# Optimization experiments

Hardware: AMD Instinct MI355X
Metric: run time of the kernel (lower is better)

Reference implementation:

```python
import jax, jax.numpy as jnp
import numpy as np

B, N, F = 64, 512, 30          # batch, pf candidates, raw features
NDIM0, NDIM = 2, 4             # coord dims: layer0 uses 2, rest use n_dim_gnn=4
NOUT, NLAYERS = 64, 5          # GNN layer width / count
NDENSE = 128
BN_EPS = 1e-3                  # keras BatchNormalization default epsilon


def setup_inputs() -> dict:
    key = jax.random.key(0)
    ks = jax.random.split(key, 20)
    xx = jax.random.normal(ks[0], (B, N, F), jnp.float32)
    # validity mask: first L_b candidates valid
    lengths = jax.random.randint(ks[1], (B,), N // 4, N + 1)
    valid = (jnp.arange(N)[None, :] < lengths[:, None]).astype(jnp.float32)
    pt = jax.random.randint(ks[2], (B, N), 0, 8).astype(jnp.float32)
    pvq = jax.random.randint(ks[3], (B, N), 0, 8).astype(jnp.float32)
    fpv = jax.random.randint(ks[4], (B, N), 0, 4).astype(jnp.float32)
    xx = xx.at[:, :, 0].set(valid).at[:, :, 27].set(pt).at[:, :, 28].set(pvq).at[:, :, 29].set(fpv)
    g = lambda k, s, sc=0.05: jax.random.normal(k, s, jnp.float32) * sc
    d_in0 = 33  # 2+2+2 embeddings + 27 float features
    return {
        "xx": xx,
        "emb1": g(ks[5], (8, 2), 0.5),
        "emb2": g(ks[6], (8, 2), 0.5),
        "emb3": g(ks[7], (4, 2), 0.5),
        "A0": g(ks[8], ((d_in0 + 1) * 2 - 1, NOUT)),   # [67,64]
        "b0": g(ks[9], (NOUT,)),
        "A_rest": g(ks[10], (NLAYERS - 1, (NOUT + 1) * 2 - 1, NOUT)),  # [4,129,64]
        "b_rest": g(ks[11], (NLAYERS - 1, NOUT)),
        "bn_gamma": jnp.ones((NLAYERS, NOUT), jnp.float32),
        "bn_beta": jnp.zeros((NLAYERS, NOUT), jnp.float32),
        "dW0": g(ks[12], (N * NOUT, NDENSE), 0.01),
        "db0": g(ks[13], (NDENSE,)),
        "dW1": g(ks[14], (NDENSE, NDENSE)),
        "db1": g(ks[15], (NDENSE,)),
        "dbn_gamma": jnp.ones((2, NDENSE), jnp.float32),
        "dbn_beta": jnp.zeros((2, NDENSE), jnp.float32),
        "W2": g(ks[16], (NDENSE, 2)),
        "b2": g(ks[17], (2,)),
    }


def _bn(x, g, b):
    # inference BatchNorm with moving_mean=0, moving_var=1 (initial stats)
    return g * x * (1.0 / jnp.sqrt(1.0 + BN_EPS)) + b


def _gnn_layer(x, mask, n_dim, A, b):
    # x: [B,N,Fin], mask: [B,N]. Original builds [B,N,N,Fin+1] via tile/reshape;
    # algebraically the reduction over senders i factorizes:
    #   ss_feat[b,j] = x[b,j] * mask[b,j] * sum_i exp(-10*d_ij)
    #   ss_last[b,j] = mask[b,j] * sum_i d_ij * exp(-10*d_ij)
    c = x[..., -n_dim:]
    diff = c[:, :, None, :] - c[:, None, :, :]      # [B,N,N,n_dim]
    dist = jnp.sum(diff * diff, axis=-1)            # [B,N,N] squared distance
    w = jnp.exp(-10.0 * dist)
    S = jnp.sum(w, axis=1)                          # [B,N] per receiver j
    T = jnp.sum(dist * w, axis=1)                   # [B,N]
    ss_feat = x * (mask * S)[..., None] - x         # subtract concat(x, 0)
    ss_last = (mask * T)[..., None]
    xcat = jnp.concatenate([x, ss_feat, ss_last], axis=-1)  # [B,N,2*Fin+1]
    return (xcat @ A + b) * mask[..., None]


def _forward(xx, emb1, emb2, emb3, A0, b0, A_rest, b_rest, bn_gamma, bn_beta,
             dW0, db0, dW1, db1, dbn_gamma, dbn_beta, W2, b2):
    mask = xx[:, :, 0]
    e1 = emb1[jnp.abs(xx[:, :, 27]).astype(jnp.int32)]
    e2 = emb2[jnp.abs(xx[:, :, 28]).astype(jnp.int32)]
    e3 = emb3[jnp.abs(xx[:, :, 29]).astype(jnp.int32)]
    x = jnp.concatenate([e1, e2, e3, xx[:, :, :27]], axis=-1)  # [B,N,33]
    x = jnp.tanh(_bn(_gnn_layer(x, mask, NDIM0, A0, b0), bn_gamma[0], bn_beta[0]))
    for k in range(NLAYERS - 1):
        x = _gnn_layer(x, mask, NDIM, A_rest[k], b_rest[k])
        x = jnp.tanh(_bn(x, bn_gamma[k + 1], bn_beta[k + 1]))
    x = x.reshape(B, N * NOUT)
    x = jax.nn.sigmoid(_bn(x @ dW0 + db0, dbn_gamma[0], dbn_beta[0]))
    x = jax.nn.sigmoid(_bn(x @ dW1 + db1, dbn_gamma[1], dbn_beta[1]))
    x = x @ W2 + b2                                  # [B,2]
    # mode == 'dm': concat zeros on the right
    return jnp.concatenate([x, jnp.zeros((B, 2), x.dtype)], axis=1)


def reference(xx, emb1, emb2, emb3, A0, b0, A_rest, b_rest, bn_gamma, bn_beta,
              dW0, db0, dW1, db1, dbn_gamma, dbn_beta, W2, b2):
    return _forward(xx, emb1, emb2, emb3, A0, b0, A_rest, b_rest, bn_gamma, bn_beta,
                    dW0, db0, dW1, db1, dbn_gamma, dbn_beta, W2, b2)
```

## Files before the change

kernel.cpp:

```cpp
#include <hip/hip_runtime.h>
#include <math.h>

#define B_ 64
#define N_ 512
#define R_ (B_*N_)
#define INV_S 0.9995003746877732f

__device__ __forceinline__ float fast_tanh(float y){
  return 1.f - 2.f*__builtin_amdgcn_rcpf(1.f + __expf(2.f*y));
}
__device__ __forceinline__ float fast_sigmoid(float v){
  return __builtin_amdgcn_rcpf(1.f + __expf(-v));
}

template<int L0>
__global__ __launch_bounds__(512, 4) void gnn_layer(
    const float* __restrict__ xx, const float* __restrict__ xin,
    const float4* __restrict__ cin, const float* __restrict__ A,
    const float* __restrict__ bias, const float* __restrict__ gamma,
    const float* __restrict__ beta,
    const float* __restrict__ emb1, const float* __restrict__ emb2,
    const float* __restrict__ emb3,
    const float* __restrict__ maskb,
    float* __restrict__ maskout,
    float4* __restrict__ cout,
    float* __restrict__ xout)
{
  constexpr int KP = L0 ? 36 : 64;
  constexpr int K  = L0 ? 33 : 64;
  __shared__ float alo[KP*64];
  __shared__ float ahi[KP*64];
  __shared__ float xl[L0 ? 64*36 : 4];
  __shared__ float spart[512], tpart[512];
  __shared__ float scl[64], tcl[64], ml[64];

  int tid = threadIdx.x;
  int jc = blockIdx.x;
  int b  = blockIdx.y;
  int rbase = b*N_, jloc = jc*64;

  if constexpr (L0){
    for (int idx = tid; idx < KP*64; idx += 512){
      int f = idx >> 6;
      alo[idx] = (f < K) ? A[idx] : 0.f;
      ahi[idx] = (f < K) ? A[(size_t)K*64 + idx] : 0.f;
    }
  } else {
    const float4* A4 = (const float4*)A;
    float4* alo4 = (float4*)alo;
    float4* ahi4 = (float4*)ahi;
    for (int idx = tid; idx < 1024; idx += 512){
      alo4[idx] = A4[idx];
      ahi4[idx] = A4[1024 + idx];
    }
  }

  if constexpr (L0){
    if (tid < 64){
      int r = rbase + jloc + tid;
      const float* row = xx + (size_t)r*30;
      float v[30];
#pragma unroll
      for (int i=0;i<30;i++) v[i] = row[i];
      int i1 = (int)fabsf(v[27]);
      int i2 = (int)fabsf(v[28]);
      int i3 = (int)fabsf(v[29]);
      float* o = &xl[tid*36];
      o[0]=emb1[i1*2+0]; o[1]=emb1[i1*2+1];
      o[2]=emb2[i2*2+0]; o[3]=emb2[i2*2+1];
      o[4]=emb3[i3*2+0]; o[5]=emb3[i3*2+1];
#pragma unroll
      for (int i=0;i<27;i++) o[6+i] = v[i];
      o[33]=0.f; o[34]=0.f; o[35]=0.f;
      ml[tid] = v[0];
      maskout[r] = v[0];
    }
  } else {
    if (tid < 64) ml[tid] = maskb[rbase + jloc + tid];
  }

  {
    int jj = tid & 63, ic = tid >> 6;
    float Ss = 0.f, Ts = 0.f;
    if constexpr (L0){
      const float* xb = xx + (size_t)rbase*30;
      float cjx = xb[(jloc+jj)*30 + 25];
      float cjy = xb[(jloc+jj)*30 + 26];
      int base = ic*64;
#pragma unroll 8
      for (int i=0;i<64;i++){
        float cix = xb[(base+i)*30 + 25];
        float ciy = xb[(base+i)*30 + 26];
        float d0 = cjx-cix, d1 = cjy-ciy;
        float dist = d0*d0 + d1*d1;
        float w = __expf(-10.f*dist);
        Ss += w; Ts += dist*w;
      }
    } else {
      const float4* cb = cin + rbase;
      float4 cj = cb[jloc + jj];
      int base = ic*64;
#pragma unroll 8
      for (int i=0;i<64;i++){
        float4 ci = cb[base+i];
        float d0 = cj.x-ci.x, d1 = cj.y-ci.y, d2 = cj.z-ci.z, d3 = cj.w-ci.w;
        float dist = d0*d0 + d1*d1 + d2*d2 + d3*d3;
        float w = __expf(-10.f*dist);
        Ss += w; Ts += dist*w;
      }
    }
    spart[tid] = Ss;
    tpart[tid] = Ts;
  }
  __syncthreads();

  if (tid < 64){
    float S = 0.f, T = 0.f;
#pragma unroll
    for (int c=0;c<8;c++){
      S += spart[tid + 64*c];
      T += tpart[tid + 64*c];
    }
    float m = ml[tid];
    scl[tid] = m*S - 1.f;
    tcl[tid] = m*T;
  }
  __syncthreads();

  int cg = tid & 15, rg = tid >> 4;
  int o0 = cg*4, lr0 = rg*2;
  const float* xb2 = xin + (size_t)(rbase + jloc)*64;
  float4 acc1[2], acc2[2];
#pragma unroll
  for (int rr=0;rr<2;rr++){
    acc1[rr] = make_float4(0.f,0.f,0.f,0.f);
    acc2[rr] = make_float4(0.f,0.f,0.f,0.f);
  }
#pragma unroll 2
  for (int kc = 0; kc < KP; kc += 4){
    float4 a1[4], a2[4], xv[2];
#pragma unroll
    for (int uu=0;uu<4;uu++){
      a1[uu] = *(const float4*)&alo[(kc+uu)*64 + o0];
      a2[uu] = *(const float4*)&ahi[(kc+uu)*64 + o0];
    }
#pragma unroll
    for (int rr=0;rr<2;rr++){
      if constexpr (L0) xv[rr] = *(const float4*)&xl[(lr0+rr)*36 + kc];
      else              xv[rr] = *(const float4*)&xb2[(lr0+rr)*64 + kc];
    }
#pragma unroll
    for (int uu=0;uu<4;uu++){
#pragma unroll
      for (int rr=0;rr<2;rr++){
        float xu = ((const float*)&xv[rr])[uu];
        acc1[rr].x = fmaf(xu, a1[uu].x, acc1[rr].x);
        acc1[rr].y = fmaf(xu, a1[uu].y, acc1[rr].y);
        acc1[rr].z = fmaf(xu, a1[uu].z, acc1[rr].z);
        acc1[rr].w = fmaf(xu, a1[uu].w, acc1[rr].w);
        acc2[rr].x = fmaf(xu, a2[uu].x, acc2[rr].x);
        acc2[rr].y = fmaf(xu, a2[uu].y, acc2[rr].y);
        acc2[rr].z = fmaf(xu, a2[uu].z, acc2[rr].z);
        acc2[rr].w = fmaf(xu, a2[uu].w, acc2[rr].w);
      }
    }
  }

  float4 alast = *(const float4*)&A[(size_t)2*K*64 + o0];
  float4 bo = *(const float4*)&bias[o0];
  float4 go = *(const float4*)&gamma[o0];
  float4 be = *(const float4*)&beta[o0];
#pragma unroll
  for (int rr=0;rr<2;rr++){
    int lr = lr0 + rr;
    int r = rbase + jloc + lr;
    float sc = scl[lr], tc = tcl[lr], m = ml[lr];
    float4 v;
    v.x = (acc1[rr].x + sc*acc2[rr].x + tc*alast.x + bo.x)*m;
    v.y = (acc1[rr].y + sc*acc2[rr].y + tc*alast.y + bo.y)*m;
    v.z = (acc1[rr].z + sc*acc2[rr].z + tc*alast.z + bo.z)*m;
    v.w = (acc1[rr].w + sc*acc2[rr].w + tc*alast.w + bo.w)*m;
    float4 t;
    t.x = fast_tanh(go.x*(v.x*INV_S) + be.x);
    t.y = fast_tanh(go.y*(v.y*INV_S) + be.y);
    t.z = fast_tanh(go.z*(v.z*INV_S) + be.z);
    t.w = fast_tanh(go.w*(v.w*INV_S) + be.w);
    *(float4*)&xout[(size_t)r*64 + o0] = t;
    if (cout && cg == 15) cout[r] = t;
  }
}

__global__ __launch_bounds__(256) void dense0_partial(
    const float* __restrict__ X, const float* __restrict__ W,
    float* __restrict__ partial)
{
  __shared__ float xt[64*32];
  __shared__ float wt[32*128];
  int tid = threadIdx.x;
  int k0 = blockIdx.x*128;
  int og = (tid & 15)*8;
  int rg = (tid >> 4)*4;
  float acc[4][8];
#pragma unroll
  for (int a=0;a<4;a++)
#pragma unroll
    for (int u=0;u<8;u++) acc[a][u]=0.f;
  for (int kt = 0; kt < 128; kt += 32){
    __syncthreads();
    for (int idx = tid; idx < 512; idx += 256){
      int r = idx >> 3, kq = idx & 7;
      *(float4*)&xt[r*32 + kq*4] =
          *(const float4*)&X[(size_t)r*32768 + k0 + kt + kq*4];
    }
    {
      const float4* Wc = (const float4*)&W[(size_t)(k0+kt)*128];
      float4* wt4 = (float4*)wt;
      for (int idx = tid; idx < 1024; idx += 256) wt4[idx] = Wc[idx];
    }
    __syncthreads();
#pragma unroll 4
    for (int k=0;k<32;k++){
      float4 w0 = *(const float4*)&wt[k*128 + og];
      float4 w1 = *(const float4*)&wt[k*128 + og + 4];
      float xs[4];
#pragma unroll
      for (int rr=0;rr<4;rr++) xs[rr] = xt[(rg+rr)*32 + k];
#pragma unroll
      for (int rr=0;rr<4;rr++){
        acc[rr][0] = fmaf(xs[rr], w0.x, acc[rr][0]);
        acc[rr][1] = fmaf(xs[rr], w0.y, acc[rr][1]);
        acc[rr][2] = fmaf(xs[rr], w0.z, acc[rr][2]);
        acc[rr][3] = fmaf(xs[rr], w0.w, acc[rr][3]);
        acc[rr][4] = fmaf(xs[rr], w1.x, acc[rr][4]);
        acc[rr][5] = fmaf(xs[rr], w1.y, acc[rr][5]);
        acc[rr][6] = fmaf(xs[rr], w1.z, acc[rr][6]);
        acc[rr][7] = fmaf(xs[rr], w1.w, acc[rr][7]);
      }
    }
  }
  float* pb = partial + (size_t)blockIdx.x*8192;
#pragma unroll
  for (int rr=0;rr<4;rr++){
    *(float4*)&pb[(rg+rr)*128 + og]     = *(float4*)&acc[rr][0];
    *(float4*)&pb[(rg+rr)*128 + og + 4] = *(float4*)&acc[rr][4];
  }
}

__global__ __launch_bounds__(256) void dense_head(
    const float* __restrict__ partial,
    const float* __restrict__ db0, const float* __restrict__ dg0,
    const float* __restrict__ dbb0,
    const float* __restrict__ dW1, const float* __restrict__ db1,
    const float* __restrict__ dg1, const float* __restrict__ dbb1,
    const float* __restrict__ W2, const float* __restrict__ b2,
    float* __restrict__ out)
{
  __shared__ float sred[256];
  __shared__ float h[128];
  __shared__ float red0[128], red1[128];
  int tid = threadIdx.x;
  int b = blockIdx.x;
  int o = tid & 127, ph = tid >> 7;
  float s = 0.f;
#pragma unroll 16
  for (int p = ph*128; p < ph*128+128; p++)
    s += partial[(size_t)p*8192 + b*128 + o];
  sred[tid] = s;
  __syncthreads();
  if (tid < 128){
    float sum = sred[tid] + sred[tid+128];
    float v = dg0[tid]*((sum + db0[tid])*INV_S) + dbb0[tid];
    h[tid] = fast_sigmoid(v);
  }
  __syncthreads();
  if (tid < 128){
    float acc = 0.f;
#pragma unroll 8
    for (int k=0;k<128;k++) acc = fmaf(h[k], dW1[k*128 + tid], acc);
    float v = dg1[tid]*((acc + db1[tid])*INV_S) + dbb1[tid];
    float h1 = fast_sigmoid(v);
    red0[tid] = h1 * W2[tid*2+0];
    red1[tid] = h1 * W2[tid*2+1];
  }
  __syncthreads();
  for (int st=64; st>0; st>>=1){
    if (tid < st){ red0[tid] += red0[tid+st]; red1[tid] += red1[tid+st]; }
    __syncthreads();
  }
  if (tid == 0){
    out[b*4+0] = red0[0] + b2[0];
    out[b*4+1] = red1[0] + b2[1];
    out[b*4+2] = 0.f;
    out[b*4+3] = 0.f;
  }
}

extern "C" void kernel_launch(void* const* d_in, const int* in_sizes, int n_in,
                              void* d_out, int out_size, void* d_ws, size_t ws_size,
                              hipStream_t stream)
{
  const float* xx   = (const float*)d_in[0];
  const float* emb1 = (const float*)d_in[1];
  const float* emb2 = (const float*)d_in[2];
  const float* emb3 = (const float*)d_in[3];
  const float* A0   = (const float*)d_in[4];
  const float* b0   = (const float*)d_in[5];
  const float* Ar   = (const float*)d_in[6];
  const float* br   = (const float*)d_in[7];
  const float* bng  = (const float*)d_in[8];
  const float* bnb  = (const float*)d_in[9];
  const float* dW0  = (const float*)d_in[10];
  const float* db0  = (const float*)d_in[11];
  const float* dW1  = (const float*)d_in[12];
  const float* db1  = (const float*)d_in[13];
  const float* dbg  = (const float*)d_in[14];
  const float* dbb  = (const float*)d_in[15];
  const float* W2   = (const float*)d_in[16];
  const float* b2   = (const float*)d_in[17];

  float* ws = (float*)d_ws;
  float*  xA      = ws;
  float*  xB      = xA + (size_t)R_*64;
  float*  partial = xB + (size_t)R_*64;
  float*  maskb   = partial + (size_t)256*8192;
  float4* cb0     = (float4*)(maskb + R_);
  float4* cb1     = cb0 + R_;

  dim3 lgrid(8, 64);
  gnn_layer<1><<<lgrid, 512, 0, stream>>>(
      xx, nullptr, nullptr, A0, b0, bng, bnb, emb1, emb2, emb3,
      nullptr, maskb, cb1, xA);
  gnn_layer<0><<<lgrid, 512, 0, stream>>>(
      xx, xA, cb1, Ar + (size_t)0*129*64, br + 0*64, bng + 64, bnb + 64,
      emb1, emb2, emb3, maskb, nullptr, cb0, xB);
  gnn_layer<0><<<lgrid, 512, 0, stream>>>(
      xx, xB, cb0, Ar + (size_t)1*129*64, br + 1*64, bng + 128, bnb + 128,
      emb1, emb2, emb3, maskb, nullptr, cb1, xA);
  gnn_layer<0><<<lgrid, 512, 0, stream>>>(
      xx, xA, cb1, Ar + (size_t)2*129*64, br + 2*64, bng + 192, bnb + 192,
      emb1, emb2, emb3, maskb, nullptr, cb0, xB);
  gnn_layer<0><<<lgrid, 512, 0, stream>>>(
      xx, xB, cb0, Ar + (size_t)3*129*64, br + 3*64, bng + 256, bnb + 256,
      emb1, emb2, emb3, maskb, nullptr, nullptr, xA);

  dense0_partial<<<256, 256, 0, stream>>>(xA, dW0, partial);
  dense_head<<<B_, 256, 0, stream>>>(partial, db0, dbg, dbb,
                                     dW1, db1, dbg + 128, dbb + 128,
                                     W2, b2, (float*)d_out);
}
```

Before: 220.4 us.

## Fuse five GNN layers into one cooperative kernel with per-batch barriers

Replaces five separate GNN layer launches with a single persistent cooperative kernel. Each block keeps its 64-row activation tile in double-buffered shared memory across layers. Only the 4-dim coordinates are exchanged through global memory, guarded by a per-batch atomic counter barrier among the 8 blocks of that batch. This removes four kernel launches and the global write/read of full 64-wide activations between layers. In exchange it adds spin-wait synchronisation, a memset launch, and larger shared memory use (about 67 KB per block), which may lower occupancy. It relies on all 512 blocks being co-resident, with a non-cooperative fallback launch that could deadlock.

Measured after the change: 281.2 us. 1.28x slower.

```diff
diff --git a/kernel.cpp b/kernel.cpp
--- a/kernel.cpp
+++ b/kernel.cpp
@@ -13,180 +13,197 @@
   return __builtin_amdgcn_rcpf(1.f + __expf(-v));
 }
 
-template<int L0>
-__global__ __launch_bounds__(512, 4) void gnn_layer(
-    const float* __restrict__ xx, const float* __restrict__ xin,
-    const float4* __restrict__ cin, const float* __restrict__ A,
-    const float* __restrict__ bias, const float* __restrict__ gamma,
-    const float* __restrict__ beta,
-    const float* __restrict__ emb1, const float* __restrict__ emb2,
-    const float* __restrict__ emb3,
-    const float* __restrict__ maskb,
-    float* __restrict__ maskout,
-    float4* __restrict__ cout,
-    float* __restrict__ xout)
+struct GnnArgs {
+  const float* xx;
+  const float* emb1; const float* emb2; const float* emb3;
+  const float* A0;  const float* b0;
+  const float* Ar;  const float* br;
+  const float* bng; const float* bnb;
+  float4* cb0; float4* cb1;
+  unsigned int* bar;
+  float* xfinal;
+};
+
+__global__ __launch_bounds__(512, 4) void gnn_fused(GnnArgs g)
 {
-  constexpr int KP = L0 ? 36 : 64;
-  constexpr int K  = L0 ? 33 : 64;
-  __shared__ float alo[KP*64];
-  __shared__ float ahi[KP*64];
-  __shared__ float xl[L0 ? 64*36 : 4];
+  __shared__ float alo[64*64];
+  __shared__ float ahi[64*64];
+  __shared__ float xsb[2][64*68];
   __shared__ float spart[512], tpart[512];
   __shared__ float scl[64], tcl[64], ml[64];
 
-  int tid = threadIdx.x;
-  int jc = blockIdx.x;
-  int b  = blockIdx.y;
-  int rbase = b*N_, jloc = jc*64;
-
-  if constexpr (L0){
-    for (int idx = tid; idx < KP*64; idx += 512){
-      int f = idx >> 6;
-      alo[idx] = (f < K) ? A[idx] : 0.f;
-      ahi[idx] = (f < K) ? A[(size_t)K*64 + idx] : 0.f;
-    }
-  } else {
-    const float4* A4 = (const float4*)A;
-    float4* alo4 = (float4*)alo;
-    float4* ahi4 = (float4*)ahi;
-    for (int idx = tid; idx < 1024; idx += 512){
-      alo4[idx] = A4[idx];
-      ahi4[idx] = A4[1024 + idx];
-    }
-  }
-
-  if constexpr (L0){
+  const int tid   = threadIdx.x;
+  const int b     = blockIdx.x;
+  const int jc    = blockIdx.y;
+  const int jloc  = jc*64;
+  const int rbase = b*N_;
+  const int cg = tid & 15, rg = tid >> 4;
+  const int o0 = cg*4,  lr0 = rg*2;
+  unsigned int* barp = g.bar + b*32;
+
+  int cur = 0;
+  for (int k = 0; k < 5; ++k){
+    const float* A;  const float* bi;  int K, KP;
+    if (k == 0){ A = g.A0;                        bi = g.b0;           K = 33; KP = 36; }
+    else       { A = g.Ar + (size_t)(k-1)*129*64; bi = g.br + (k-1)*64; K = 64; KP = 64; }
+    const float* gam = g.bng + k*64;
+    const float* bet = g.bnb + k*64;
+
+    if (k == 0){
+      for (int idx = tid; idx < 36*64; idx += 512){
+        int f = idx >> 6;
+        alo[idx] = (f < 33) ? A[idx] : 0.f;
+        ahi[idx] = (f < 33) ? A[33*64 + idx] : 0.f;
+      }
+      if (tid < 64){
+        const float* row = g.xx + (size_t)(rbase + jloc + tid)*30;
+        float v[30];
+#pragma unroll
+        for (int i=0;i<30;i++) v[i] = row[i];
+        int i1 = (int)fabsf(v[27]);
+        int i2 = (int)fabsf(v[28]);
+        int i3 = (int)fabsf(v[29]);
+        float* o = &xsb[0][tid*68];
+        o[0]=g.emb1[i1*2+0]; o[1]=g.emb1[i1*2+1];
+        o[2]=g.emb2[i2*2+0]; o[3]=g.emb2[i2*2+1];
+        o[4]=g.emb3[i3*2+0]; o[5]=g.emb3[i3*2+1];
+#pragma unroll
+        for (int i=0;i<27;i++) o[6+i] = v[i];
+        o[33]=0.f; o[34]=0.f; o[35]=0.f;
+        ml[tid] = v[0];
+      }
+    } else {
+      __syncthreads();
+      if (tid == 0){
+        __builtin_amdgcn_fence(__ATOMIC_RELEASE, "agent");
+        __hip_atomic_fetch_add(barp, 1u, __ATOMIC_RELAXED, __HIP_MEMORY_SCOPE_AGENT);
+      }
+      {
+        const float4* A4 = (const float4*)A;
+        float4* alo4 = (float4*)alo;
+        float4* ahi4 = (float4*)ahi;
+        for (int idx = tid; idx < 1024; idx += 512){
+          alo4[idx] = A4[idx];
+          ahi4[idx] = A4[1024 + idx];
+        }
+      }
+      if (tid == 0){
+        unsigned int tgt = 8u*(unsigned int)k;
+        while (__hip_atomic_load(barp, __ATOMIC_RELAXED, __HIP_MEMORY_SCOPE_AGENT) < tgt)
+          __builtin_amdgcn_s_sleep(2);
+        __builtin_amdgcn_fence(__ATOMIC_ACQUIRE, "agent");
+      }
+      __syncthreads();
+    }
+
+    {
+      int jj = tid & 63, ic = tid >> 6, base = ic*64;
+      float Ss = 0.f, Ts = 0.f;
+      if (k == 0){
+        const float* xb = g.xx + (size_t)rbase*30;
+        float cjx = xb[(jloc+jj)*30 + 25];
+        float cjy = xb[(jloc+jj)*30 + 26];
+#pragma unroll 8
+        for (int i=0;i<64;i++){
+          float cix = xb[(base+i)*30 + 25];
+          float ciy = xb[(base+i)*30 + 26];
+          float d0 = cjx-cix, d1 = cjy-ciy;
+          float dist = d0*d0 + d1*d1;
+          float w = __expf(-10.f*dist);
+          Ss += w; Ts += dist*w;
+        }
+      } else {
+        const float4* cbr = ((k & 1) ? g.cb0 : g.cb1) + rbase;
+        float4 cj = *(const float4*)&xsb[cur][jj*68 + 60];
+#pragma unroll 8
+        for (int i=0;i<64;i++){
+          float4 ci = cbr[base+i];
+          float d0 = cj.x-ci.x, d1 = cj.y-ci.y, d2 = cj.z-ci.z, d3 = cj.w-ci.w;
+          float dist = d0*d0 + d1*d1 + d2*d2 + d3*d3;
+          float w = __expf(-10.f*dist);
+          Ss += w; Ts += dist*w;
+        }
+      }
+      spart[tid] = Ss;
+      tpart[tid] = Ts;
+    }
+    __syncthreads();
+
     if (tid < 64){
-      int r = rbase + jloc + tid;
-      const float* row = xx + (size_t)r*30;
-      float v[30];
-#pragma unroll
-      for (int i=0;i<30;i++) v[i] = row[i];
-      int i1 = (int)fabsf(v[27]);
-      int i2 = (int)fabsf(v[28]);
-      int i3 = (int)fabsf(v[29]);
-      float* o = &xl[tid*36];
-      o[0]=emb1[i1*2+0]; o[1]=emb1[i1*2+1];
-      o[2]=emb2[i2*2+0]; o[3]=emb2[i2*2+1];
-      o[4]=emb3[i3*2+0]; o[5]=emb3[i3*2+1];
-#pragma unroll
-      for (int i=0;i<27;i++) o[6+i] = v[i];
-      o[33]=0.f; o[34]=0.f; o[35]=0.f;
-      ml[tid] = v[0];
-      maskout[r] = v[0];
-    }
-  } else {
-    if (tid < 64) ml[tid] = maskb[rbase + jloc + tid];
-  }
-
-  {
-    int jj = tid & 63, ic = tid >> 6;
-    float Ss = 0.f, Ts = 0.f;
-    if constexpr (L0){
-      const float* xb = xx + (size_t)rbase*30;
-      float cjx = xb[(jloc+jj)*30 + 25];
-      float cjy = xb[(jloc+jj)*30 + 26];
-      int base = ic*64;
-#pragma unroll 8
-      for (int i=0;i<64;i++){
-        float cix = xb[(base+i)*30 + 25];
-        float ciy = xb[(base+i)*30 + 26];
-        float d0 = cjx-cix, d1 = cjy-ciy;
-        float dist = d0*d0 + d1*d1;
-        float w = __expf(-10.f*dist);
-        Ss += w; Ts += dist*w;
-      }
-    } else {
-      const float4* cb = cin + rbase;
-      float4 cj = cb[jloc + jj];
-      int base = ic*64;
-#pragma unroll 8
-      for (int i=0;i<64;i++){
-        float4 ci = cb[base+i];
-        float d0 = cj.x-ci.x, d1 = cj.y-ci.y, d2 = cj.z-ci.z, d3 = cj.w-ci.w;
-        float dist = d0*d0 + d1*d1 + d2*d2 + d3*d3;
-        float w = __expf(-10.f*dist);
-        Ss += w; Ts += dist*w;
-      }
-    }
-    spart[tid] = Ss;
-    tpart[tid] = Ts;
-  }
-  __syncthreads();
-
-  if (tid < 64){
-    float S = 0.f, T = 0.f;
-#pragma unroll
-    for (int c=0;c<8;c++){
-      S += spart[tid + 64*c];
-      T += tpart[tid + 64*c];
-    }
-    float m = ml[tid];
-    scl[tid] = m*S - 1.f;
-    tcl[tid] = m*T;
-  }
-  __syncthreads();
-
-  int cg = tid & 15, rg = tid >> 4;
-  int o0 = cg*4, lr0 = rg*2;
-  const float* xb2 = xin + (size_t)(rbase + jloc)*64;
-  float4 acc1[2], acc2[2];
-#pragma unroll
-  for (int rr=0;rr<2;rr++){
-    acc1[rr] = make_float4(0.f,0.f,0.f,0.f);
-    acc2[rr] = make_float4(0.f,0.f,0.f,0.f);
-  }
+      float S = 0.f, T = 0.f;
+#pragma unroll
+      for (int c=0;c<8;c++){
+        S += spart[tid + 64*c];
+        T += tpart[tid + 64*c];
+      }
+      float m = ml[tid];
+      scl[tid] = m*S - 1.f;
+      tcl[tid] = m*T;
+    }
+    __syncthreads();
+
+    const float* xsrc = &xsb[cur][0];
+    float4 acc1[2], acc2[2];
+#pragma unroll
+    for (int rr=0;rr<2;rr++){
+      acc1[rr] = make_float4(0.f,0.f,0.f,0.f);
+      acc2[rr] = make_float4(0.f,0.f,0.f,0.f);
+    }
 #pragma unroll 2
-  for (int kc = 0; kc < KP; kc += 4){
-    float4 a1[4], a2[4], xv[2];
-#pragma unroll
-    for (int uu=0;uu<4;uu++){
-      a1[uu] = *(const float4*)&alo[(kc+uu)*64 + o0];
-      a2[uu] = *(const float4*)&ahi[(kc+uu)*64 + o0];
-    }
+    for (int kc = 0; kc < KP; kc += 4){
+      float4 a1[4], a2[4], xv[2];
+#pragma unroll
+      for (int uu=0;uu<4;uu++){
+        a1[uu] = *(const float4*)&alo[(kc+uu)*64 + o0];
+        a2[uu] = *(const float4*)&ahi[(kc+uu)*64 + o0];
+      }
+#pragma unroll
+      for (int rr=0;rr<2;rr++)
+        xv[rr] = *(const float4*)&xsrc[(lr0+rr)*68 + kc];
+#pragma unroll
+      for (int uu=0;uu<4;uu++){
+#pragma unroll
+        for (int rr=0;rr<2;rr++){
+          float xu = ((const float*)&xv[rr])[uu];
+          acc1[rr].x = fmaf(xu, a1[uu].x, acc1[rr].x);
+          acc1[rr].y = fmaf(xu, a1[uu].y, acc1[rr].y);
+          acc1[rr].z = fmaf(xu, a1[uu].z, acc1[rr].z);
+          acc1[rr].w = fmaf(xu, a1[uu].w, acc1[rr].w);
+          acc2[rr].x = fmaf(xu, a2[uu].x, acc2[rr].x);
+          acc2[rr].y = fmaf(xu, a2[uu].y, acc2[rr].y);
+          acc2[rr].z = fmaf(xu, a2[uu].z, acc2[rr].z);
+          acc2[rr].w = fmaf(xu, a2[uu].w, acc2[rr].w);
+        }
+      }
+    }
+
+    float4 alast = *(const float4*)&A[(size_t)2*K*64 + o0];
+    float4 bo = *(const float4*)&bi[o0];
+    float4 go = *(const float4*)&gam[o0];
+    float4 bb = *(const float4*)&bet[o0];
+    float4* cbw = (k & 1) ? g.cb1 : g.cb0;
 #pragma unroll
     for (int rr=0;rr<2;rr++){
-      if constexpr (L0) xv[rr] = *(const float4*)&xl[(lr0+rr)*36 + kc];
-      else              xv[rr] = *(const float4*)&xb2[(lr0+rr)*64 + kc];
-    }
-#pragma unroll
-    for (int uu=0;uu<4;uu++){
-#pragma unroll
-      for (int rr=0;rr<2;rr++){
-        float xu = ((const float*)&xv[rr])[uu];
-        acc1[rr].x = fmaf(xu, a1[uu].x, acc1[rr].x);
-        acc1[rr].y = fmaf(xu, a1[uu].y, acc1[rr].y);
-        acc1[rr].z = fmaf(xu, a1[uu].z, acc1[rr].z);
-        acc1[rr].w = fmaf(xu, a1[uu].w, acc1[rr].w);
-        acc2[rr].x = fmaf(xu, a2[uu].x, acc2[rr].x);
-        acc2[rr].y = fmaf(xu, a2[uu].y, acc2[rr].y);
-        acc2[rr].z = fmaf(xu, a2[uu].z, acc2[rr].z);
-        acc2[rr].w = fmaf(xu, a2[uu].w, acc2[rr].w);
-      }
-    }
-  }
-
-  float4 alast = *(const float4*)&A[(size_t)2*K*64 + o0];
-  float4 bo = *(const float4*)&bias[o0];
-  float4 go = *(const float4*)&gamma[o0];
-  float4 be = *(const float4*)&beta[o0];
-#pragma unroll
-  for (int rr=0;rr<2;rr++){
-    int lr = lr0 + rr;
-    int r = rbase + jloc + lr;
-    float sc = scl[lr], tc = tcl[lr], m = ml[lr];
-    float4 v;
-    v.x = (acc1[rr].x + sc*acc2[rr].x + tc*alast.x + bo.x)*m;
-    v.y = (acc1[rr].y + sc*acc2[rr].y + tc*alast.y + bo.y)*m;
-    v.z = (acc1[rr].z + sc*acc2[rr].z + tc*alast.z + bo.z)*m;
-    v.w = (acc1[rr].w + sc*acc2[rr].w + tc*alast.w + bo.w)*m;
-    float4 t;
-    t.x = fast_tanh(go.x*(v.x*INV_S) + be.x);
-    t.y = fast_tanh(go.y*(v.y*INV_S) + be.y);
-    t.z = fast_tanh(go.z*(v.z*INV_S) + be.z);
-    t.w = fast_tanh(go.w*(v.w*INV_S) + be.w);
-    *(float4*)&xout[(size_t)r*64 + o0] = t;
-    if (cout && cg == 15) cout[r] = t;
+      int lr = lr0 + rr;
+      float sc = scl[lr], tc = tcl[lr], m = ml[lr];
+      float4 v;
+      v.x = (acc1[rr].x + sc*acc2[rr].x + tc*alast.x + bo.x)*m;
+      v.y = (acc1[rr].y + sc*acc2[rr].y + tc*alast.y + bo.y)*m;
+      v.z = (acc1[rr].z + sc*acc2[rr].z + tc*alast.z + bo.z)*m;
+      v.w = (acc1[rr].w + sc*acc2[rr].w + tc*alast.w + bo.w)*m;
+      float4 t;
+      t.x = fast_tanh(go.x*(v.x*INV_S) + bb.x);
+      t.y = fast_tanh(go.y*(v.y*INV_S) + bb.y);
+      t.z = fast_tanh(go.z*(v.z*INV_S) + bb.z);
+      t.w = fast_tanh(go.w*(v.w*INV_S) + bb.w);
+      if (k < 4){
+        *(float4*)&xsb[cur^1][lr*68 + o0] = t;
+        if (cg == 15) cbw[rbase + jloc + lr] = t;
+      } else {
+        *(float4*)&g.xfinal[(size_t)(rbase + jloc + lr)*64 + o0] = t;
+      }
+    }
+    cur ^= 1;
   }
 }
 
@@ -320,28 +337,24 @@
 
   float* ws = (float*)d_ws;
   float*  xA      = ws;
-  float*  xB      = xA + (size_t)R_*64;
-  float*  partial = xB + (size_t)R_*64;
-  float*  maskb   = partial + (size_t)256*8192;
-  float4* cb0     = (float4*)(maskb + R_);
+  float*  partial = xA + (size_t)R_*64;
+  float4* cb0     = (float4*)(partial + (size_t)256*8192);
   float4* cb1     = cb0 + R_;
-
-  dim3 lgrid(8, 64);
-  gnn_layer<1><<<lgrid, 512, 0, stream>>>(
-      xx, nullptr, nullptr, A0, b0, bng, bnb, emb1, emb2, emb3,
-      nullptr, maskb, cb1, xA);
-  gnn_layer<0><<<lgrid, 512, 0, stream>>>(
-      xx, xA, cb1, Ar + (size_t)0*129*64, br + 0*64, bng + 64, bnb + 64,
-      emb1, emb2, emb3, maskb, nullptr, cb0, xB);
-  gnn_layer<0><<<lgrid, 512, 0, stream>>>(
-      xx, xB, cb0, Ar + (size_t)1*129*64, br + 1*64, bng + 128, bnb + 128,
-      emb1, emb2, emb3, maskb, nullptr, cb1, xA);
-  gnn_layer<0><<<lgrid, 512, 0, stream>>>(
-      xx, xA, cb1, Ar + (size_t)2*129*64, br + 2*64, bng + 192, bnb + 192,
-      emb1, emb2, emb3, maskb, nullptr, cb0, xB);
-  gnn_layer<0><<<lgrid, 512, 0, stream>>>(
-      xx, xB, cb0, Ar + (size_t)3*129*64, br + 3*64, bng + 256, bnb + 256,
-      emb1, emb2, emb3, maskb, nullptr, nullptr, xA);
+  unsigned int* bar = (unsigned int*)(cb1 + R_);
+
+  hipMemsetAsync(bar, 0, 64*32*sizeof(unsigned int), stream);
+
+  GnnArgs ga;
+  ga.xx = xx; ga.emb1 = emb1; ga.emb2 = emb2; ga.emb3 = emb3;
+  ga.A0 = A0; ga.b0 = b0; ga.Ar = Ar; ga.br = br;
+  ga.bng = bng; ga.bnb = bnb;
+  ga.cb0 = cb0; ga.cb1 = cb1; ga.bar = bar; ga.xfinal = xA;
+
+  void* kargs[] = { (void*)&ga };
+  if (hipLaunchCooperativeKernel((void*)gnn_fused, dim3(64,8), dim3(512),
+                                 kargs, 0, stream) != hipSuccess){
+    hipLaunchKernelGGL(gnn_fused, dim3(64,8), dim3(512), 0, stream, ga);
+  }
 
   dense0_partial<<<256, 256, 0, stream>>>(xA, dW0, partial);
   dense_head<<<B_, 256, 0, stream>>>(partial, db0, dbg, dbb,
```
